# Performance work log

Measured on AMD Instinct MI355X. Metric: run time of the kernel, lower is better.

Reference implementation:

```python
import jax, jax.numpy as jnp
import numpy as np

KERNEL_SIZES = [2, 4, 8, 16, 32, 64]
MAXK = max(k + k // 2 for k in KERNEL_SIZES[1:])  # 96
PAD_LO = (MAXK - 1) // 2  # 47
PAD_HI = MAXK - 1 - PAD_LO  # 48


def _alternating(K, even_negative):
    f = np.ones(K, np.float32)
    idx = np.arange(K)
    mask = (idx % 2 == 0) if even_negative else (idx % 2 == 1)
    f[mask] = -1.0
    return f


def make_weight_bank():
    """Builds all 17 fixed filters, zero-padded and center-aligned into one
    (17, 1, MAXK) bank so a single 'same'-padded conv matches 17 torch convs.
    Alignment: torch pads left=(K-1)//2 for kernel K; embedding each kernel at
    offset (MAXK-1)//2 - (K-1)//2 inside a MAXK kernel padded (PAD_LO, PAD_HI)
    reproduces the identical output."""
    filters = []
    for K in KERNEL_SIZES:              # group 1: -1 at even indices
        filters.append(_alternating(K, True))
    for K in KERNEL_SIZES:              # group 2: -1 at odd indices
        filters.append(_alternating(K, False))
    for K in KERNEL_SIZES[1:]:          # group 3: piecewise quadratic, len K + K//2
        q = K // 4
        left = (np.linspace(0.0, 1.0, q + 1, dtype=np.float32)[1:]) ** 2
        right = left[::-1]
        filters.append(np.concatenate([-left, -right, 2 * left, 2 * right, -left, -right]).astype(np.float32))
    W = np.zeros((len(filters), 1, MAXK), np.float32)
    for i, f in enumerate(filters):
        K = len(f)
        o = (MAXK - 1) // 2 - (K - 1) // 2
        W[i, 0, o:o + K] = f
    return jnp.asarray(W)


def setup_inputs() -> dict:
    key = jax.random.key(0)
    x = jax.random.normal(key, (128, 1, 32768), dtype=jnp.float32)
    W = make_weight_bank()  # (17, 1, 96), fixed non-trainable filters
    return {"x": x, "W": W}


def reference(x, W):
    # x: (B, 1, L); W: (17, 1, MAXK). One cross-correlation conv = bank of 17
    # 'same'-padded conv1d filters; then ReLU.
    y = jax.lax.conv_general_dilated(
        x, W,
        window_strides=(1,),
        padding=[(PAD_LO, PAD_HI)],
        dimension_numbers=("NCH", "OIH", "NCH"),
    )
    return jax.nn.relu(y)  # (B, 17, L)
```

## Files before the change

kernel.cpp:

```cpp
#include <hip/hip_runtime.h>


#define S_LEN   32768
#define NFILT   17
#define TILE    1024
#define HALO_L  47
#define WIN     (TILE + 96)
#define NCHUNK  (WIN / 8)
#define PITCH   284
#define NTHREADS 256

template<int Q>
__device__ __forceinline__ float third_w(int j) {
    constexpr float inv = 1.0f / (float)Q;
    const int seg = j / Q;
    const int i = j - seg * Q;
    const float t = (seg == 0 || seg == 2 || seg == 4) ? (float)(i + 1) * inv
                                                       : (float)(Q - i) * inv;
    const float v = t * t;
    return (seg == 2 || seg == 3) ? 2.0f * v : -v;
}

template<int K>
__device__ __forceinline__ float4 third_acc(const float* __restrict__ xsp, int tid) {
    constexpr int Q    = K / 4;
    constexpr int SPAN = 6 * Q;
    constexpr int C    = (3 * K / 2 - 1) / 2;
    float a0 = 0.f, a1 = 0.f, a2 = 0.f, a3 = 0.f;
#pragma unroll
    for (int u = 0; u < SPAN + 3; ++u) {
        const int d = (HALO_L - C) + u;
        const float xv = xsp[(d & 3) * PITCH + tid + (d >> 2)];
        if (u < SPAN)               a0 = fmaf(third_w<Q>(u),     xv, a0);
        if (u >= 1 && u - 1 < SPAN) a1 = fmaf(third_w<Q>(u - 1), xv, a1);
        if (u >= 2 && u - 2 < SPAN) a2 = fmaf(third_w<Q>(u - 2), xv, a2);
        if (u >= 3 && u - 3 < SPAN) a3 = fmaf(third_w<Q>(u - 3), xv, a3);
    }
    return make_float4(a0, a1, a2, a3);
}

template<int K>
__device__ __forceinline__ float4 alt_acc(const float* __restrict__ Qsp, int tid) {
    constexpr int H = (K - 1) / 2;
    float v[4];
#pragma unroll
    for (int r = 0; r < 4; ++r) {
        const int d  = HALO_L + r - H;
        const int d2 = d + K;
        const float qa = Qsp[(d  & 3) * PITCH + tid + (d  >> 2)];
        const float qb = Qsp[(d2 & 3) * PITCH + tid + (d2 >> 2)];
        const float dd = qb - qa;
        v[r] = (d & 1) ? dd : -dd;
    }
    return make_float4(v[0], v[1], v[2], v[3]);
}

__global__ __launch_bounds__(NTHREADS)
void conv_bank_kernel(const float* __restrict__ x, float* __restrict__ out) {
    __shared__ float xsp[4 * PITCH];
    __shared__ float Qsp[4 * PITCH];
    __shared__ float scanb[NTHREADS];

    const int tid = threadIdx.x;
    const int ts  = blockIdx.x * TILE;
    const int b   = blockIdx.y;
    const float* __restrict__ xrow = x + (size_t)b * S_LEN;

    for (int j = tid; j < WIN; j += NTHREADS) {
        const int g = ts - HALO_L + j;
        float v = 0.f;
        if ((unsigned)g < (unsigned)S_LEN) v = xrow[g];
        xsp[(j & 3) * PITCH + (j >> 2)] = v;
    }
    __syncthreads();

    float csum = 0.f;
    if (tid < NCHUNK) {
#pragma unroll
        for (int k = 0; k < 8; ++k) {
            const float v = xsp[(k & 3) * PITCH + 2 * tid + (k >> 2)];
            csum += (k & 1) ? -v : v;
        }
    }
    scanb[tid] = csum;
    __syncthreads();
    float incl = csum;
#pragma unroll
    for (int off = 1; off < NTHREADS; off <<= 1) {
        const float add = (tid >= off) ? scanb[tid - off] : 0.f;
        __syncthreads();
        incl += add;
        scanb[tid] = incl;
        __syncthreads();
    }
    if (tid < NCHUNK) {
        float run = incl - csum;
#pragma unroll
        for (int k = 0; k < 8; ++k) {
            const int idx = (k & 3) * PITCH + 2 * tid + (k >> 2);
            Qsp[idx] = run;
            const float v = xsp[idx];
            run += (k & 1) ? -v : v;
        }
        if (tid == NCHUNK - 1) Qsp[WIN >> 2] = run;
    }
    __syncthreads();

    const int t0 = ts + 4 * tid;
    float* __restrict__ obase = out + (size_t)b * NFILT * S_LEN + t0;

    auto store_relu = [&](int j, float4 v) {
        float4 s;
        s.x = fmaxf(v.x, 0.f); s.y = fmaxf(v.y, 0.f);
        s.z = fmaxf(v.z, 0.f); s.w = fmaxf(v.w, 0.f);
        *reinterpret_cast<float4*>(obase + (size_t)j * S_LEN) = s;
    };
    auto store_pair = [&](int j, float4 a) {
        store_relu(j, a);
        store_relu(j + 6, make_float4(-a.x, -a.y, -a.z, -a.w));
    };

    store_pair(0, alt_acc<2 >(Qsp, tid));
    store_pair(1, alt_acc<4 >(Qsp, tid));
    store_pair(2, alt_acc<8 >(Qsp, tid));
    store_pair(3, alt_acc<16>(Qsp, tid));
    store_pair(4, alt_acc<32>(Qsp, tid));
    store_pair(5, alt_acc<64>(Qsp, tid));

    store_relu(12, third_acc<4 >(xsp, tid));
    store_relu(13, third_acc<8 >(xsp, tid));
    store_relu(14, third_acc<16>(xsp, tid));
    store_relu(15, third_acc<32>(xsp, tid));
    store_relu(16, third_acc<64>(xsp, tid));
}

extern "C" void kernel_launch(void* const* d_in, const int* in_sizes, int n_in,
                              void* d_out, int out_size, void* d_ws, size_t ws_size,
                              hipStream_t stream) {
    const float* x = (const float*)d_in[0];
    float* out = (float*)d_out;
    const int nbatch = in_sizes[0] / S_LEN;
    dim3 grid(S_LEN / TILE, nbatch, 1);
    conv_bank_kernel<<<grid, NTHREADS, 0, stream>>>(x, out);
}
```

Measured before the change: 298.5 us.

## Replace prefix-sum scheme with direct register-blocked convolution using compile-time weights

The old kernel handled the alternating filters with a block-wide scan over shared memory, using many barriers, and read the quadratic filters' taps one scalar shared load at a time. The new kernel drops the scan. Every thread loads float4 chunks of the tile and accumulates all 11 distinct filters for its 4 outputs with fully unrolled FMAs. The weights come from a constexpr table, so zero taps are skipped at compile time. This removes the barriers and most shared-memory load traffic, at the cost of more arithmetic on the alternating filters and 44 live accumulators per thread.

```diff
diff --git a/kernel.cpp b/kernel.cpp
--- a/kernel.cpp
+++ b/kernel.cpp
@@ -1,137 +1,107 @@
 #include <hip/hip_runtime.h>
 
 
-#define S_LEN   32768
-#define NFILT   17
-#define TILE    1024
-#define HALO_L  47
-#define WIN     (TILE + 96)
-#define NCHUNK  (WIN / 8)
-#define PITCH   284
+#define S_LEN    32768
+#define NFILT    17
+#define TILE     1024
+#define HALO_L   47
+#define WIN      (TILE + 96)
 #define NTHREADS 256
+#define NCHUNKS  25
 
-template<int Q>
-__device__ __forceinline__ float third_w(int j) {
-    constexpr float inv = 1.0f / (float)Q;
-    const int seg = j / Q;
-    const int i = j - seg * Q;
-    const float t = (seg == 0 || seg == 2 || seg == 4) ? (float)(i + 1) * inv
-                                                       : (float)(Q - i) * inv;
-    const float v = t * t;
-    return (seg == 2 || seg == 3) ? 2.0f * v : -v;
-}
-
-template<int K>
-__device__ __forceinline__ float4 third_acc(const float* __restrict__ xsp, int tid) {
-    constexpr int Q    = K / 4;
-    constexpr int SPAN = 6 * Q;
-    constexpr int C    = (3 * K / 2 - 1) / 2;
-    float a0 = 0.f, a1 = 0.f, a2 = 0.f, a3 = 0.f;
-#pragma unroll
-    for (int u = 0; u < SPAN + 3; ++u) {
-        const int d = (HALO_L - C) + u;
-        const float xv = xsp[(d & 3) * PITCH + tid + (d >> 2)];
-        if (u < SPAN)               a0 = fmaf(third_w<Q>(u),     xv, a0);
-        if (u >= 1 && u - 1 < SPAN) a1 = fmaf(third_w<Q>(u - 1), xv, a1);
-        if (u >= 2 && u - 2 < SPAN) a2 = fmaf(third_w<Q>(u - 2), xv, a2);
-        if (u >= 3 && u - 3 < SPAN) a3 = fmaf(third_w<Q>(u - 3), xv, a3);
+struct BankT {
+    float w[11][96];
+    constexpr BankT() : w{} {
+        const int KS[6] = {2, 4, 8, 16, 32, 64};
+        for (int fi = 0; fi < 6; ++fi) {
+            const int K = KS[fi];
+            const int o = 47 - (K - 1) / 2;
+            for (int i = 0; i < K; ++i)
+                w[fi][o + i] = (i % 2 == 0) ? -1.0f : 1.0f;
+        }
+        for (int fi = 0; fi < 5; ++fi) {
+            const int K = KS[fi + 1];
+            const int Q = K / 4;
+            const int o = 47 - (3 * K / 2 - 1) / 2;
+            for (int j = 0; j < 6 * Q; ++j) {
+                const int seg = j / Q, i = j - seg * Q;
+                const float t = (seg == 0 || seg == 2 || seg == 4)
+                                ? (float)(i + 1) / (float)Q
+                                : (float)(Q - i) / (float)Q;
+                const float v = t * t;
+                w[fi + 6][o + j] = (seg == 2 || seg == 3) ? 2.0f * v : -v;
+            }
+        }
     }
-    return make_float4(a0, a1, a2, a3);
-}
-
-template<int K>
-__device__ __forceinline__ float4 alt_acc(const float* __restrict__ Qsp, int tid) {
-    constexpr int H = (K - 1) / 2;
-    float v[4];
-#pragma unroll
-    for (int r = 0; r < 4; ++r) {
-        const int d  = HALO_L + r - H;
-        const int d2 = d + K;
-        const float qa = Qsp[(d  & 3) * PITCH + tid + (d  >> 2)];
-        const float qb = Qsp[(d2 & 3) * PITCH + tid + (d2 >> 2)];
-        const float dd = qb - qa;
-        v[r] = (d & 1) ? dd : -dd;
-    }
-    return make_float4(v[0], v[1], v[2], v[3]);
-}
+};
+__constant__ constexpr BankT BANK;
 
 __global__ __launch_bounds__(NTHREADS)
 void conv_bank_kernel(const float* __restrict__ x, float* __restrict__ out) {
-    __shared__ float xsp[4 * PITCH];
-    __shared__ float Qsp[4 * PITCH];
-    __shared__ float scanb[NTHREADS];
+    __shared__ float xs[WIN];
 
     const int tid = threadIdx.x;
     const int ts  = blockIdx.x * TILE;
     const int b   = blockIdx.y;
     const float* __restrict__ xrow = x + (size_t)b * S_LEN;
 
-    for (int j = tid; j < WIN; j += NTHREADS) {
-        const int g = ts - HALO_L + j;
-        float v = 0.f;
-        if ((unsigned)g < (unsigned)S_LEN) v = xrow[g];
-        xsp[(j & 3) * PITCH + (j >> 2)] = v;
+#pragma unroll
+    for (int j0 = 0; j0 < WIN; j0 += NTHREADS) {
+        const int j = j0 + tid;
+        if (j0 + NTHREADS <= WIN || j < WIN) {
+            const int g = ts - HALO_L + j;
+            xs[j] = ((unsigned)g < (unsigned)S_LEN) ? xrow[g] : 0.0f;
+        }
     }
     __syncthreads();
 
-    float csum = 0.f;
-    if (tid < NCHUNK) {
+    float acc[11][4];
 #pragma unroll
-        for (int k = 0; k < 8; ++k) {
-            const float v = xsp[(k & 3) * PITCH + 2 * tid + (k >> 2)];
-            csum += (k & 1) ? -v : v;
+    for (int f = 0; f < 11; ++f)
+#pragma unroll
+        for (int r = 0; r < 4; ++r) acc[f][r] = 0.0f;
+
+    const float4* __restrict__ xv4 = reinterpret_cast<const float4*>(xs) + tid;
+#pragma unroll
+    for (int c = 0; c < NCHUNKS; ++c) {
+        const float4 xq = xv4[c];
+        const float xe[4] = {xq.x, xq.y, xq.z, xq.w};
+#pragma unroll
+        for (int l = 0; l < 4; ++l) {
+            const int d = 4 * c + l;
+#pragma unroll
+            for (int r = 0; r < 4; ++r) {
+                const int k = d - r;
+                if (k >= 0 && k < 96) {
+#pragma unroll
+                    for (int f = 0; f < 11; ++f) {
+                        const float wv = BANK.w[f][k];
+                        if (wv != 0.0f)
+                            acc[f][r] = fmaf(wv, xe[l], acc[f][r]);
+                    }
+                }
+            }
         }
     }
-    scanb[tid] = csum;
-    __syncthreads();
-    float incl = csum;
-#pragma unroll
-    for (int off = 1; off < NTHREADS; off <<= 1) {
-        const float add = (tid >= off) ? scanb[tid - off] : 0.f;
-        __syncthreads();
-        incl += add;
-        scanb[tid] = incl;
-        __syncthreads();
-    }
-    if (tid < NCHUNK) {
-        float run = incl - csum;
-#pragma unroll
-        for (int k = 0; k < 8; ++k) {
-            const int idx = (k & 3) * PITCH + 2 * tid + (k >> 2);
-            Qsp[idx] = run;
-            const float v = xsp[idx];
-            run += (k & 1) ? -v : v;
-        }
-        if (tid == NCHUNK - 1) Qsp[WIN >> 2] = run;
-    }
-    __syncthreads();
 
     const int t0 = ts + 4 * tid;
     float* __restrict__ obase = out + (size_t)b * NFILT * S_LEN + t0;
 
-    auto store_relu = [&](int j, float4 v) {
-        float4 s;
-        s.x = fmaxf(v.x, 0.f); s.y = fmaxf(v.y, 0.f);
-        s.z = fmaxf(v.z, 0.f); s.w = fmaxf(v.w, 0.f);
-        *reinterpret_cast<float4*>(obase + (size_t)j * S_LEN) = s;
-    };
-    auto store_pair = [&](int j, float4 a) {
-        store_relu(j, a);
-        store_relu(j + 6, make_float4(-a.x, -a.y, -a.z, -a.w));
+    auto store_relu = [&](int row, float a0, float a1, float a2, float a3) {
+        const float4 s = make_float4(fmaxf(a0, 0.f), fmaxf(a1, 0.f),
+                                     fmaxf(a2, 0.f), fmaxf(a3, 0.f));
+        *reinterpret_cast<float4*>(obase + (size_t)row * S_LEN) = s;
     };
 
-    store_pair(0, alt_acc<2 >(Qsp, tid));
-    store_pair(1, alt_acc<4 >(Qsp, tid));
-    store_pair(2, alt_acc<8 >(Qsp, tid));
-    store_pair(3, alt_acc<16>(Qsp, tid));
-    store_pair(4, alt_acc<32>(Qsp, tid));
-    store_pair(5, alt_acc<64>(Qsp, tid));
-
-    store_relu(12, third_acc<4 >(xsp, tid));
-    store_relu(13, third_acc<8 >(xsp, tid));
-    store_relu(14, third_acc<16>(xsp, tid));
-    store_relu(15, third_acc<32>(xsp, tid));
-    store_relu(16, third_acc<64>(xsp, tid));
+#pragma unroll
+    for (int f = 0; f < 6; ++f) {
+        store_relu(f,      acc[f][0],  acc[f][1],  acc[f][2],  acc[f][3]);
+        store_relu(f + 6, -acc[f][0], -acc[f][1], -acc[f][2], -acc[f][3]);
+    }
+#pragma unroll
+    for (int f = 0; f < 5; ++f)
+        store_relu(12 + f, acc[6 + f][0], acc[6 + f][1],
+                           acc[6 + f][2], acc[6 + f][3]);
 }
 
 extern "C" void kernel_launch(void* const* d_in, const int* in_sizes, int n_in,
```

Result: slower. 306.2 us (+2.6%).
